# Kernel optimization log

Hardware: AMD Instinct MI355X
Metric: run time of the kernel (lower is better)

The kernel has to match this reference:

```python
import jax, jax.numpy as jnp
import numpy as np

B, N, M, DQ, DK, DV, H = 8, 1024, 1024, 512, 512, 512, 8
DH = DV // H           # per-head dim (dim_split)
DFF = 4 * DV           # FFN hidden dim
EPS = 1e-5


def _layernorm(x, g, b):
    mu = jnp.mean(x, axis=-1, keepdims=True)
    var = jnp.mean(jnp.square(x - mu), axis=-1, keepdims=True)
    return (x - mu) * jax.lax.rsqrt(var + EPS) * g + b


def setup_inputs() -> dict:
    key = jax.random.key(0)
    ks = jax.random.split(key, 20)
    s = 0.02
    return {
        "Q": jax.random.normal(ks[0], (B, N, DQ), jnp.float32),
        "K": jax.random.normal(ks[1], (B, M, DK), jnp.float32),
        "Wq": jax.random.normal(ks[2], (DV, DQ), jnp.float32) * s,
        "bq": jnp.zeros((DV,), jnp.float32),
        "Wk": jax.random.normal(ks[3], (DV, DK), jnp.float32) * s,
        "bk": jnp.zeros((DV,), jnp.float32),
        "Wv": jax.random.normal(ks[4], (DV, DK), jnp.float32) * s,
        "bv": jnp.zeros((DV,), jnp.float32),
        "W1": jax.random.normal(ks[5], (DFF, DV), jnp.float32) * s,
        "b1": jnp.zeros((DFF,), jnp.float32),
        "W2": jax.random.normal(ks[6], (DFF, DFF), jnp.float32) * s,
        "b2": jnp.zeros((DFF,), jnp.float32),
        "W3": jax.random.normal(ks[7], (DV, DFF), jnp.float32) * s,
        "b3": jnp.zeros((DV,), jnp.float32),
        "g0": jnp.ones((DV,), jnp.float32),
        "beta0": jnp.zeros((DV,), jnp.float32),
        "g1": jnp.ones((DV,), jnp.float32),
        "beta1": jnp.zeros((DV,), jnp.float32),
    }


def reference(Q, K, Wq, bq, Wk, bk, Wv, bv, W1, b1, W2, b2, W3, b3, g0, beta0, g1, beta1):
    # projections (torch Linear: x @ W.T + b)
    Qp = Q @ Wq.T + bq            # [B, N, DV]
    Kp = K @ Wk.T + bk            # [B, M, DV]
    Vp = K @ Wv.T + bv            # [B, M, DV]

    # split heads: [B, S, DV] -> [B, S, H, DH]
    Qh = Qp.reshape(B, N, H, DH)
    Kh = Kp.reshape(B, M, H, DH)
    Vh = Vp.reshape(B, M, H, DH)

    # scaled dot-product attention (scale = sqrt(head_dim))
    A = jnp.einsum("bnhd,bmhd->bhnm", Qh, Kh) / jnp.sqrt(jnp.float32(DH))
    A = jax.nn.softmax(A, axis=-1)
    O = jnp.einsum("bhnm,bmhd->bnhd", A, Vh).reshape(B, N, DV)

    # residual with projected Q, then LN
    O = _layernorm(O + Qp, g0, beta0)

    # FFN: Linear->ReLU->Linear->ReLU->Linear (num_hidden_layers=2)
    h = jax.nn.relu(O @ W1.T + b1)
    h = jax.nn.relu(h @ W2.T + b2)
    Off = h @ W3.T + b3

    return _layernorm(O + Off, g1, beta1)
```

## Files before the change

### kernel.cpp

```cpp
#include <hip/hip_runtime.h>


typedef __bf16 bf16_t;
typedef __bf16 bf16x8 __attribute__((ext_vector_type(8)));
typedef __bf16 bf16x4 __attribute__((ext_vector_type(4)));
typedef __bf16 bf16x2 __attribute__((ext_vector_type(2)));
typedef float  f32x4  __attribute__((ext_vector_type(4)));
typedef float  f32x16 __attribute__((ext_vector_type(16)));
typedef int    i32x4_t __attribute__((ext_vector_type(4)));
typedef int    i32x8_t __attribute__((ext_vector_type(8)));

__device__ __forceinline__ f32x4 mfma16(bf16x8 a, bf16x8 b, f32x4 c) {
  return __builtin_amdgcn_mfma_f32_16x16x32_bf16(a, b, c, 0, 0, 0);
}

__device__ __forceinline__ void gload_lds16(const void* g, void* l) {
  __builtin_amdgcn_global_load_lds((const __attribute__((address_space(1))) void*)g,
                                   (__attribute__((address_space(3))) void*)l,
                                   16, 0, 0);
}

__device__ __forceinline__ unsigned char to_fp8(float v) {
  return (unsigned char)(__builtin_amdgcn_cvt_pk_fp8_f32(v, v, 0, false) & 0xff);
}

__global__ __launch_bounds__(256) void cast_all(
    const float* __restrict__ Q, const float* __restrict__ K,
    const float* __restrict__ Wq, const float* __restrict__ Wk,
    const float* __restrict__ Wv, const float* __restrict__ W1,
    const float* __restrict__ W2, const float* __restrict__ W3,
    bf16_t* Qb, bf16_t* Kb, bf16_t* Wqb, bf16_t* Wkb, bf16_t* Wvb,
    unsigned char* W1q, unsigned char* W2q, unsigned char* W3q)
{
  long i = ((long)blockIdx.x * 256 + threadIdx.x) * 4;
  if (i >= 9175040L) {
    const float* s; unsigned char* d; long o;
    if      (i < 10223616L) { s = W1; d = W1q; o = i - 9175040L;  }
    else if (i < 14417920L) { s = W2; d = W2q; o = i - 10223616L; }
    else                    { s = W3; d = W3q; o = i - 14417920L; }
    float4 v = *(const float4*)(s + o);
    unsigned int lo = __builtin_amdgcn_cvt_pk_fp8_f32(v.x, v.y, 0, false);
    unsigned int hi = __builtin_amdgcn_cvt_pk_fp8_f32(v.z, v.w, 0, false);
    *(unsigned int*)(d + o) = (lo & 0xffffu) | (hi << 16);
    return;
  }
  const float* s; bf16_t* d; long o;
  if      (i <  4194304L) { s = Q;  d = Qb;  o = i;             }
  else if (i <  8388608L) { s = K;  d = Kb;  o = i - 4194304L;  }
  else if (i <  8650752L) { s = Wq; d = Wqb; o = i - 8388608L;  }
  else if (i <  8912896L) { s = Wk; d = Wkb; o = i - 8650752L;  }
  else                    { s = Wv; d = Wvb; o = i - 8912896L;  }
  float4 v = *(const float4*)(s + o);
  bf16x4 w;
  w[0] = (bf16_t)v.x; w[1] = (bf16_t)v.y; w[2] = (bf16_t)v.z; w[3] = (bf16_t)v.w;
  *(bf16x4*)(d + o) = w;
}

template <bool VTEPI>
__device__ __forceinline__ void gemm_core(
    const bf16_t* __restrict__ A, const bf16_t* __restrict__ W,
    const float* __restrict__ bias,
    bf16_t* __restrict__ Cb, bf16_t* __restrict__ VTout,
    float bscale, int N, int K, int lda, int ldb, int bx, int by)
{
  constexpr int FI = 4;
  constexpr int FJ = 4;
  constexpr int CN = 64;
  constexpr int SM_AB = 256 * 64 * 2;
  constexpr int SM_TS = 128 * 132 * 2;
  constexpr int SMEM = (VTEPI && SM_TS > SM_AB) ? SM_TS : SM_AB;

  __shared__ __align__(16) char smem[SMEM];

  const int tid  = threadIdx.x;
  const int wave = tid >> 6, lane = tid & 63;
  const int lq   = lane & 15, quad = lane >> 4;
  const int wm   = wave & 1;
  const int wn   = wave >> 1;
  const long row0 = (long)bx * 128;
  const long col0 = (long)by * 128;

  const int sr = tid >> 3;
  const int cg = (tid & 7) ^ (sr & 7);
  const bf16_t* ag = A + (row0 + sr) * (long)lda + cg * 8;
  const bf16_t* bg = W + (col0 + sr) * (long)ldb + cg * 8;
  const int asOff = wave * 1024;
  const int bsOff = 128 * 128 + wave * 1024;
  const long arows32 = 32L * lda;
  const long brows32 = 32L * ldb;

  auto stage = [&](int k0) {
#pragma unroll
    for (int is = 0; is < 4; is++)
      gload_lds16(ag + is * arows32 + k0, smem + asOff + is * 4096);
#pragma unroll
    for (int is = 0; is < 4; is++)
      gload_lds16(bg + is * brows32 + k0, smem + bsOff + is * 4096);
  };

  const int off0 = (quad ^ (lq & 7)) * 8;
  const int aO0 = ((wm * 64 + lq) * 64 + off0) * 2;
  const int aO1 = ((wm * 64 + lq) * 64 + (off0 ^ 32)) * 2;
  const int bO0 = 128 * 128 + ((wn * CN + lq) * 64 + off0) * 2;
  const int bO1 = 128 * 128 + ((wn * CN + lq) * 64 + (off0 ^ 32)) * 2;

  f32x4 acc[FI][FJ];
#pragma unroll
  for (int i = 0; i < FI; i++)
#pragma unroll
    for (int j = 0; j < FJ; j++) acc[i][j] = (f32x4){0.f, 0.f, 0.f, 0.f};

  const int nt = K >> 6;
  for (int t = 0; t < nt; ++t) {
    __syncthreads();
    stage(t * 64);
    __syncthreads();

    bf16x8 af[FI], bw[FJ];
#pragma unroll
    for (int i = 0; i < FI; i++) af[i] = *(const bf16x8*)(smem + aO0 + i * 2048);
#pragma unroll
    for (int j = 0; j < FJ; j++) bw[j] = *(const bf16x8*)(smem + bO0 + j * 2048);
#pragma unroll
    for (int i = 0; i < FI; i++)
#pragma unroll
      for (int j = 0; j < FJ; j++)
        acc[i][j] = mfma16(af[i], bw[j], acc[i][j]);
#pragma unroll
    for (int i = 0; i < FI; i++) af[i] = *(const bf16x8*)(smem + aO1 + i * 2048);
#pragma unroll
    for (int j = 0; j < FJ; j++) bw[j] = *(const bf16x8*)(smem + bO1 + j * 2048);
#pragma unroll
    for (int i = 0; i < FI; i++)
#pragma unroll
      for (int j = 0; j < FJ; j++)
        acc[i][j] = mfma16(af[i], bw[j], acc[i][j]);
  }

  float bc[FJ];
#pragma unroll
  for (int j = 0; j < FJ; j++)
    bc[j] = bias ? bias[col0 + wn * CN + j * 16 + lq] : 0.f;

  if (VTEPI && VTout) {
    bf16_t* Ts = (bf16_t*)smem;
    __syncthreads();
#pragma unroll
    for (int i = 0; i < FI; i++)
#pragma unroll
      for (int j = 0; j < FJ; j++) {
        bf16x4 pv;
#pragma unroll
        for (int r = 0; r < 4; r++) pv[r] = (bf16_t)(acc[i][j][r] + bc[j]);
        *(bf16x4*)(Ts + (wn * CN + j * 16 + lq) * 132 + wm * 64 + i * 16 + quad * 4) = pv;
      }
    __syncthreads();
    const int b  = bx >> 3;
    const int mb = (bx & 7) * 128;
    const int h0 = by * 2;
    const int dd = tid >> 4;
    const int mc = (tid & 15) * 8;
#pragma unroll
    for (int p = 0; p < 8; p++) {
      const int d = dd + p * 16;
      bf16x8 v = *(const bf16x8*)(Ts + d * 132 + mc);
      *(bf16x8*)(VTout + ((long)(b * 8 + h0 + (d >> 6))) * 65536
                 + (d & 63) * 1024 + mb + mc) = v;
    }
    return;
  }

  const long rb = row0 + wm * 64 + quad * 4;
  const long cb = col0 + wn * CN + lq;
#pragma unroll
  for (int i = 0; i < FI; i++)
#pragma unroll
    for (int j = 0; j < FJ; j++)
#pragma unroll
      for (int r = 0; r < 4; r++) {
        float v = acc[i][j][r] + bc[j];
        long idx = (rb + i * 16 + r) * (long)N + cb + j * 16;
        if (Cb) Cb[idx] = (bf16_t)(v * bscale);
      }
}

__global__ __launch_bounds__(256) void proj3(
    const bf16_t* __restrict__ Qb, const bf16_t* __restrict__ Kb,
    const bf16_t* __restrict__ Wqb, const bf16_t* __restrict__ Wkb,
    const bf16_t* __restrict__ Wvb,
    const float* __restrict__ bq, const float* __restrict__ bk,
    const float* __restrict__ bv,
    bf16_t* Qpb, bf16_t* Kpb, bf16_t* VT)
{
  const int z = blockIdx.z;
  const bf16_t* A  = (z == 0) ? Qb : Kb;
  const bf16_t* Wt = (z == 0) ? Wqb : ((z == 1) ? Wkb : Wvb);
  const float* bias = (z == 0) ? bq : ((z == 1) ? bk : bv);
  bf16_t* Cb = (z == 0) ? Qpb : ((z == 1) ? Kpb : nullptr);
  bf16_t* VTout = (z == 2) ? VT : nullptr;
  const float sc = (z == 1) ? 0.125f : 1.0f;
  gemm_core<true>(A, Wt, bias, Cb, VTout, sc,
                  512, 512, 512, 512, blockIdx.x, blockIdx.y);
}

template <int OUT, int BN>
__device__ __forceinline__ void fp8_gemm_core(
    const unsigned char* __restrict__ A, const unsigned char* __restrict__ B,
    const float* __restrict__ bias, unsigned char* __restrict__ C8,
    bf16_t* __restrict__ Cb, int ldab, int K, int koff, int N,
    int bxi, int byi)
{
  constexpr int NT = 2 * BN;
  constexpr int RPP = NT / 8;
  constexpr int A_P = 128 / RPP;
  constexpr int B_P = BN / RPP;
  constexpr int PASSB = NT * 16;

  __shared__ unsigned char As[16384];
  __shared__ unsigned char Bs[BN * 128];
  const int tid = threadIdx.x;
  const int wave = tid >> 6, lane = tid & 63;
  const int wm = wave & 1, wn = wave >> 1;
  const int m = lane & 31, h = lane >> 5;
  const long row0 = (long)bxi * 128;
  const long col0 = (long)byi * BN;

  const int sr = tid >> 3;
  const int cg = (tid & 7) ^ (sr & 7);
  const unsigned char* ag = A + (row0 + sr) * (long)ldab + koff + cg * 16;
  const unsigned char* bg = B + (col0 + sr) * (long)ldab + koff + cg * 16;
  char* asD = (char*)As + wave * 1024;
  char* bsD = (char*)Bs + wave * 1024;
  const long rowsPP = (long)RPP * ldab;

  const int ar0 = wm * 64 + m, ar1 = ar0 + 32;
  const int br0 = wn * 64 + m, br1 = wn * 64 + 32 + m;

  f32x16 acc[2][2];
#pragma unroll
  for (int mi = 0; mi < 2; mi++)
#pragma unroll
    for (int nj = 0; nj < 2; nj++)
#pragma unroll
      for (int r = 0; r < 16; r++) acc[mi][nj][r] = 0.f;

  for (int k0 = 0; k0 < K; k0 += 128) {
    __syncthreads();
#pragma unroll
    for (int is = 0; is < A_P; is++)
      gload_lds16(ag + is * rowsPP + k0, asD + is * PASSB);
#pragma unroll
    for (int is = 0; is < B_P; is++)
      gload_lds16(bg + is * rowsPP + k0, bsD + is * PASSB);
    __syncthreads();
#pragma unroll
    for (int ks = 0; ks < 2; ks++) {
      const int c0 = ks * 4 + h * 2;
      i32x8_t a[2], b[2];
#pragma unroll
      for (int mi = 0; mi < 2; mi++) {
        const int r = mi ? ar1 : ar0;
        i32x4_t lo = *(const i32x4_t*)(As + r * 128 + ((c0    ) ^ (r & 7)) * 16);
        i32x4_t hi = *(const i32x4_t*)(As + r * 128 + ((c0 + 1) ^ (r & 7)) * 16);
        a[mi][0] = lo[0]; a[mi][1] = lo[1]; a[mi][2] = lo[2]; a[mi][3] = lo[3];
        a[mi][4] = hi[0]; a[mi][5] = hi[1]; a[mi][6] = hi[2]; a[mi][7] = hi[3];
      }
#pragma unroll
      for (int nj = 0; nj < 2; nj++) {
        const int r = nj ? br1 : br0;
        i32x4_t lo = *(const i32x4_t*)(Bs + r * 128 + ((c0    ) ^ (r & 7)) * 16);
        i32x4_t hi = *(const i32x4_t*)(Bs + r * 128 + ((c0 + 1) ^ (r & 7)) * 16);
        b[nj][0] = lo[0]; b[nj][1] = lo[1]; b[nj][2] = lo[2]; b[nj][3] = lo[3];
        b[nj][4] = hi[0]; b[nj][5] = hi[1]; b[nj][6] = hi[2]; b[nj][7] = hi[3];
      }
#pragma unroll
      for (int mi = 0; mi < 2; mi++)
#pragma unroll
        for (int nj = 0; nj < 2; nj++)
          acc[mi][nj] = __builtin_amdgcn_mfma_scale_f32_32x32x64_f8f6f4(
              a[mi], b[nj], acc[mi][nj], 0, 0,
              0, 0x7f7f7f7f, 0, 0x7f7f7f7f);
    }
  }

  float bc[2];
  bc[0] = bias ? bias[col0 + wn * 64 + m] : 0.f;
  bc[1] = bias ? bias[col0 + wn * 64 + 32 + m] : 0.f;
#pragma unroll
  for (int mi = 0; mi < 2; mi++)
#pragma unroll
    for (int nj = 0; nj < 2; nj++)
#pragma unroll
      for (int reg = 0; reg < 16; reg++) {
        const int rl = (reg & 3) + 8 * (reg >> 2) + 4 * h;
        const long idx = (row0 + wm * 64 + mi * 32 + rl) * (long)N
                       + col0 + wn * 64 + nj * 32 + m;
        if (OUT == 0) {
          float v = fmaxf(acc[mi][nj][reg] + bc[nj], 0.f);
          C8[idx] = to_fp8(v);
        } else {
          Cb[idx] = (bf16_t)acc[mi][nj][reg];
        }
      }
}

__global__ __launch_bounds__(512) void ffn1_fp8(
    const unsigned char* __restrict__ Xq, const unsigned char* __restrict__ W1,
    const float* __restrict__ bias, unsigned char* __restrict__ C)
{
  fp8_gemm_core<0, 256>(Xq, W1, bias, C, nullptr, 512, 512, 0, 2048,
                        blockIdx.x, blockIdx.y);
}

__global__ __launch_bounds__(512) void ffn2_fp8(
    const unsigned char* __restrict__ H1, const unsigned char* __restrict__ W2,
    const float* __restrict__ bias, unsigned char* __restrict__ C)
{
  fp8_gemm_core<0, 256>(H1, W2, bias, C, nullptr, 2048, 2048, 0, 2048,
                        blockIdx.x, blockIdx.y);
}

__global__ __launch_bounds__(256) void ffn3_fp8(
    const unsigned char* __restrict__ H2, const unsigned char* __restrict__ W3,
    bf16_t* __restrict__ Off01)
{
  const int z = blockIdx.z;
  fp8_gemm_core<1, 128>(H2, W3, nullptr, nullptr, Off01 + (long)z * 4194304,
                        2048, 1024, z * 1024, 512, blockIdx.x, blockIdx.y);
}

__global__ __launch_bounds__(256) void attn(
    const bf16_t* __restrict__ Qp, const bf16_t* __restrict__ Kp,
    const bf16_t* __restrict__ VT, bf16_t* __restrict__ O)
{
  const int d0 = blockIdx.x;
  const int j  = d0 >> 3;
  const int g  = (d0 & 7) * 8 + (j >> 3);
  const int qb = j & 7;
  const int h  = g & 7, b = g >> 3;

  const int tid = threadIdx.x;
  const int wave = tid >> 6, lane = tid & 63;
  const int lq = lane & 15, quad = lane >> 4;

  __shared__ bf16_t Ks[2][8192];
  __shared__ bf16_t VTs[2][8192];
  __shared__ bf16_t Ps[4][16 * 72];

  const long bh = (long)b * 1024;
  const int qrowA = qb * 128 + wave * 16 + lq;
  const int qrowB = qrowA + 64;

  const bf16_t* qpA = Qp + (bh + qrowA) * 512 + h * 64 + quad * 8;
  const bf16_t* qpB = Qp + (bh + qrowB) * 512 + h * 64 + quad * 8;
  const bf16x8 qfA0 = *(const bf16x8*)qpA;
  const bf16x8 qfA1 = *(const bf16x8*)(qpA + 32);
  const bf16x8 qfB0 = *(const bf16x8*)qpB;
  const bf16x8 qfB1 = *(const bf16x8*)(qpB + 32);

  f32x4 oaccA[4], oaccB[4];
#pragma unroll
  for (int t = 0; t < 4; t++) {
    oaccA[t] = (f32x4){0.f, 0.f, 0.f, 0.f};
    oaccB[t] = (f32x4){0.f, 0.f, 0.f, 0.f};
  }
  float lA = 0.f, lB = 0.f;

  const int sr = tid >> 3;
  const int cg = (tid & 7) ^ (sr & 7);
  const bf16_t* kg  = Kp + bh * 512 + h * 64;
  const bf16_t* vtg = VT + ((long)b * 8 + h) * 65536;
  const int off0 = (quad ^ (lq & 7)) * 8;

  auto stage = [&](int m0, int bi) {
    char* ksDst = (char*)(Ks[bi]) + wave * 1024;
    char* vtDst = (char*)(VTs[bi]) + wave * 1024;
#pragma unroll
    for (int s = 0; s < 2; s++) {
      gload_lds16(kg + (long)(m0 + s * 64 + sr) * 512 + cg * 8,      ksDst + s * 8192);
      gload_lds16(kg + (long)(m0 + s * 64 + sr + 32) * 512 + cg * 8, ksDst + s * 8192 + 4096);
      gload_lds16(vtg + (long)sr * 1024 + m0 + s * 64 + cg * 8,        vtDst + s * 8192);
      gload_lds16(vtg + (long)(sr + 32) * 1024 + m0 + s * 64 + cg * 8, vtDst + s * 8192 + 4096);
    }
  };

  stage(0, 0);

  for (int t = 0; t < 8; ++t) {
    const int cur = t & 1;
    if (t < 7) {
      stage((t + 1) * 128, cur ^ 1);
      asm volatile("s_waitcnt vmcnt(8)" ::: "memory");
    } else {
      asm volatile("s_waitcnt vmcnt(0)" ::: "memory");
    }
    __builtin_amdgcn_s_barrier();
    __builtin_amdgcn_sched_barrier(0);

    const bf16_t* Kc = Ks[cur];
    const bf16_t* Vc = VTs[cur];

    f32x4 stA[8], stB[8];
#pragma unroll
    for (int tt = 0; tt < 8; tt++) {
      const bf16_t* kb = Kc + (tt >> 2) * 4096 + ((tt & 3) * 16 + lq) * 64;
      bf16x8 ka0 = *(const bf16x8*)(kb + off0);
      bf16x8 ka1 = *(const bf16x8*)(kb + (off0 ^ 32));
      f32x4 sA = (f32x4){0.f, 0.f, 0.f, 0.f};
      sA = mfma16(ka0, qfA0, sA);
      sA = mfma16(ka1, qfA1, sA);
      stA[tt] = sA;
      f32x4 sB = (f32x4){0.f, 0.f, 0.f, 0.f};
      sB = mfma16(ka0, qfB0, sB);
      sB = mfma16(ka1, qfB1, sB);
      stB[tt] = sB;
    }

    float lsA = 0.f, lsB = 0.f;
#pragma unroll
    for (int tt = 0; tt < 8; tt++)
#pragma unroll
      for (int r = 0; r < 4; r++) {
        float pA = __expf(stA[tt][r]);
        stA[tt][r] = pA;
        lsA += pA;
        float pB = __expf(stB[tt][r]);
        stB[tt][r] = pB;
        lsB += pB;
      }
    lsA += __shfl_xor(lsA, 16, 64);
    lsA += __shfl_xor(lsA, 32, 64);
    lA += lsA;
    lsB += __shfl_xor(lsB, 16, 64);
    lsB += __shfl_xor(lsB, 32, 64);
    lB += lsB;

    bf16_t* pw = &Ps[wave][0];
#pragma unroll
    for (int hh = 0; hh < 2; hh++) {
#pragma unroll
      for (int tt = 0; tt < 4; tt++) {
        bf16x4 pv;
#pragma unroll
        for (int r = 0; r < 4; r++) pv[r] = (bf16_t)stA[hh * 4 + tt][r];
        *(bf16x4*)(pw + lq * 72 + tt * 16 + quad * 4) = pv;
      }
#pragma unroll
      for (int ks = 0; ks < 2; ks++) {
        bf16x8 pb = *(const bf16x8*)(pw + lq * 72 + ks * 32 + quad * 8);
#pragma unroll
        for (int dt = 0; dt < 4; dt++) {
          const bf16_t* vb = Vc + hh * 4096 + (dt * 16 + lq) * 64;
          bf16x8 va = *(const bf16x8*)(vb + (ks ? (off0 ^ 32) : off0));
          oaccA[dt] = mfma16(va, pb, oaccA[dt]);
        }
      }
    }
#pragma unroll
    for (int hh = 0; hh < 2; hh++) {
#pragma unroll
      for (int tt = 0; tt < 4; tt++) {
        bf16x4 pv;
#pragma unroll
        for (int r = 0; r < 4; r++) pv[r] = (bf16_t)stB[hh * 4 + tt][r];
        *(bf16x4*)(pw + lq * 72 + tt * 16 + quad * 4) = pv;
      }
#pragma unroll
      for (int ks = 0; ks < 2; ks++) {
        bf16x8 pb = *(const bf16x8*)(pw + lq * 72 + ks * 32 + quad * 8);
#pragma unroll
        for (int dt = 0; dt < 4; dt++) {
          const bf16_t* vb = Vc + hh * 4096 + (dt * 16 + lq) * 64;
          bf16x8 va = *(const bf16x8*)(vb + (ks ? (off0 ^ 32) : off0));
          oaccB[dt] = mfma16(va, pb, oaccB[dt]);
        }
      }
    }

    __builtin_amdgcn_sched_barrier(0);
    __builtin_amdgcn_s_barrier();
  }

  const float invA = 1.f / lA;
  const float invB = 1.f / lB;
  bf16_t* opA = O + (bh + qrowA) * 512 + h * 64 + quad * 4;
  bf16_t* opB = O + (bh + qrowB) * 512 + h * 64 + quad * 4;
#pragma unroll
  for (int dt = 0; dt < 4; dt++) {
    bf16x4 vA, vB;
#pragma unroll
    for (int r = 0; r < 4; r++) {
      vA[r] = (bf16_t)(oaccA[dt][r] * invA);
      vB[r] = (bf16_t)(oaccB[dt][r] * invB);
    }
    *(bf16x4*)(opA + dt * 16) = vA;
    *(bf16x4*)(opB + dt * 16) = vB;
  }
}

__device__ __forceinline__ float2 ld2(const float* p, long row, int tid) {
  return ((const float2*)(p + row * 512))[tid];
}
__device__ __forceinline__ float2 ld2(const bf16_t* p, long row, int tid) {
  bf16x2 v = *(const bf16x2*)(p + row * 512 + tid * 2);
  return make_float2((float)v[0], (float)v[1]);
}

__device__ __forceinline__ void ln_finish(
    float x0, float x1, const float* g, const float* be, int tid,
    int wave, int lane, float* of, bf16_t* ob, unsigned char* o8, long row)
{
  float s = x0 + x1, ss = x0 * x0 + x1 * x1;
#pragma unroll
  for (int off = 1; off < 64; off <<= 1) {
    s  += __shfl_xor(s,  off, 64);
    ss += __shfl_xor(ss, off, 64);
  }
  __shared__ float sm[8];
  if (lane == 0) { sm[wave] = s; sm[4 + wave] = ss; }
  __syncthreads();
  s  = sm[0] + sm[1] + sm[2] + sm[3];
  ss = sm[4] + sm[5] + sm[6] + sm[7];
  const float mu = s * (1.f / 512.f);
  const float var = ss * (1.f / 512.f) - mu * mu;
  const float rs = rsqrtf(var + 1e-5f);
  const float2 gg = ((const float2*)g)[tid];
  const float2 bb = ((const float2*)be)[tid];
  const float o0 = (x0 - mu) * rs * gg.x + bb.x;
  const float o1 = (x1 - mu) * rs * gg.y + bb.y;
  if (of) ((float2*)(of + row * 512))[tid] = make_float2(o0, o1);
  if (ob) {
    bf16x2 t; t[0] = (bf16_t)o0; t[1] = (bf16_t)o1;
    *(bf16x2*)(ob + row * 512 + tid * 2) = t;
  }
  if (o8) {
    unsigned int p = __builtin_amdgcn_cvt_pk_fp8_f32(o0, o1, 0, false);
    *(unsigned short*)(o8 + row * 512 + tid * 2) = (unsigned short)(p & 0xffffu);
  }
}

__global__ __launch_bounds__(256) void ln_res(
    const bf16_t* __restrict__ A, const bf16_t* __restrict__ Bv,
    const float* __restrict__ g, const float* __restrict__ be,
    bf16_t* __restrict__ ob, unsigned char* __restrict__ o8)
{
  const int row = blockIdx.x, tid = threadIdx.x;
  const float2 va = ld2(A,  (long)row, tid);
  const float2 vb = ld2(Bv, (long)row, tid);
  ln_finish(va.x + vb.x, va.y + vb.y, g, be, tid, tid >> 6, tid & 63,
            nullptr, ob, o8, row);
}

__global__ __launch_bounds__(256) void ln_res3(
    const bf16_t* __restrict__ X, const bf16_t* __restrict__ O0,
    const bf16_t* __restrict__ O1, const float* __restrict__ bias,
    const float* __restrict__ g, const float* __restrict__ be,
    float* __restrict__ of)
{
  const int row = blockIdx.x, tid = threadIdx.x;
  const float2 vx = ld2(X,  (long)row, tid);
  const float2 v0 = ld2(O0, (long)row, tid);
  const float2 v1 = ld2(O1, (long)row, tid);
  const float2 vb = ((const float2*)bias)[tid];
  ln_finish(vx.x + v0.x + v1.x + vb.x, vx.y + v0.y + v1.y + vb.y,
            g, be, tid, tid >> 6, tid & 63, of, nullptr, nullptr, row);
}

extern "C" void kernel_launch(void* const* d_in, const int* in_sizes, int n_in,
                              void* d_out, int out_size, void* d_ws, size_t ws_size,
                              hipStream_t stream)
{
  const float* Q   = (const float*)d_in[0];
  const float* K   = (const float*)d_in[1];
  const float* Wq  = (const float*)d_in[2];
  const float* bq  = (const float*)d_in[3];
  const float* Wk  = (const float*)d_in[4];
  const float* bk  = (const float*)d_in[5];
  const float* Wv  = (const float*)d_in[6];
  const float* bv  = (const float*)d_in[7];
  const float* W1  = (const float*)d_in[8];
  const float* b1  = (const float*)d_in[9];
  const float* W2  = (const float*)d_in[10];
  const float* b2  = (const float*)d_in[11];
  const float* W3  = (const float*)d_in[12];
  const float* b3  = (const float*)d_in[13];
  const float* g0  = (const float*)d_in[14];
  const float* be0 = (const float*)d_in[15];
  const float* g1  = (const float*)d_in[16];
  const float* be1 = (const float*)d_in[17];

  char* ws = (char*)d_ws;
  bf16_t* Wqb = (bf16_t*)(ws + 0);
  bf16_t* Wkb = (bf16_t*)(ws + 524288);
  bf16_t* Wvb = (bf16_t*)(ws + 1048576);
  unsigned char* W1q = (unsigned char*)(ws + 1572864);
  unsigned char* W3q = (unsigned char*)(ws + 3670016);
  unsigned char* W2q = (unsigned char*)(ws + 5767168);
  bf16_t* Qb  = (bf16_t*)(ws + 14155776);
  bf16_t* Kb  = (bf16_t*)(ws + 22544384);
  bf16_t* Qpb = (bf16_t*)(ws + 30932992);
  bf16_t* Kpb = (bf16_t*)(ws + 39321600);
  bf16_t* VT  = (bf16_t*)(ws + 47710208);
  bf16_t* Of  = (bf16_t*)(ws + 14155776);
  bf16_t* Xb  = (bf16_t*)(ws + 22544384);
  unsigned char* Xq = (unsigned char*)(ws + 47710208);
  unsigned char* H2q = (unsigned char*)(ws + 30932992);
  unsigned char* H1q = (unsigned char*)(ws + 64487424);
  bf16_t* Off0 = (bf16_t*)(ws + 64487424);
  bf16_t* Off1 = (bf16_t*)(ws + 72876032);
  float*  out = (float*)d_out;

  cast_all<<<15104, 256, 0, stream>>>(Q, K, Wq, Wk, Wv, W1, W2, W3,
                                      Qb, Kb, Wqb, Wkb, Wvb, W1q, W2q, W3q);
  proj3<<<dim3(64, 4, 3), 256, 0, stream>>>(Qb, Kb, Wqb, Wkb, Wvb, bq, bk, bv,
                                            Qpb, Kpb, VT);
  attn<<<dim3(512, 1, 1), 256, 0, stream>>>(Qpb, Kpb, VT, Of);
  ln_res<<<8192, 256, 0, stream>>>(Of, Qpb, g0, be0, Xb, Xq);
  ffn1_fp8<<<dim3(64, 8), 512, 0, stream>>>(Xq, W1q, b1, H1q);
  ffn2_fp8<<<dim3(64, 8), 512, 0, stream>>>(H1q, W2q, b2, H2q);
  ffn3_fp8<<<dim3(64, 4, 2), 256, 0, stream>>>(H2q, W3q, Off0);
  ln_res3<<<8192, 256, 0, stream>>>(Xb, Off0, Off1, b3, g1, be1, out);
}
```

Baseline: 257.3 us.

## Double-buffer bf16 projection GEMM LDS staging and retile FFN1 to 128-column blocks

The bf16 GEMM core (used by the projections) now keeps two LDS buffers. It prefetches the next K-tile with global_load_lds while the current tile is consumed, and uses explicit vmcnt waits and barriers instead of two syncthreads per iteration. This aims to overlap global loads with MFMA work, at the cost of double the shared memory per block, which may reduce occupancy. Separately, FFN1 switches to a 128-wide tile with 256 threads and twice as many column blocks, for finer granularity on the small-K GEMM.

```diff
diff --git a/kernel.cpp b/kernel.cpp
--- a/kernel.cpp
+++ b/kernel.cpp
@@ -67,8 +67,7 @@
   constexpr int FJ = 4;
   constexpr int CN = 64;
   constexpr int SM_AB = 256 * 64 * 2;
-  constexpr int SM_TS = 128 * 132 * 2;
-  constexpr int SMEM = (VTEPI && SM_TS > SM_AB) ? SM_TS : SM_AB;
+  constexpr int SMEM = 2 * SM_AB;
 
   __shared__ __align__(16) char smem[SMEM];
 
@@ -89,13 +88,14 @@
   const long arows32 = 32L * lda;
   const long brows32 = 32L * ldb;
 
-  auto stage = [&](int k0) {
+  auto stage = [&](int k0, int bi) {
+    char* base = smem + bi * SM_AB;
 #pragma unroll
     for (int is = 0; is < 4; is++)
-      gload_lds16(ag + is * arows32 + k0, smem + asOff + is * 4096);
+      gload_lds16(ag + is * arows32 + k0, base + asOff + is * 4096);
 #pragma unroll
     for (int is = 0; is < 4; is++)
-      gload_lds16(bg + is * brows32 + k0, smem + bsOff + is * 4096);
+      gload_lds16(bg + is * brows32 + k0, base + bsOff + is * 4096);
   };
 
   const int off0 = (quad ^ (lq & 7)) * 8;
@@ -111,30 +111,41 @@
     for (int j = 0; j < FJ; j++) acc[i][j] = (f32x4){0.f, 0.f, 0.f, 0.f};
 
   const int nt = K >> 6;
+  stage(0, 0);
   for (int t = 0; t < nt; ++t) {
-    __syncthreads();
-    stage(t * 64);
-    __syncthreads();
+    const int cur = t & 1;
+    if (t < nt - 1) {
+      stage((t + 1) * 64, cur ^ 1);
+      asm volatile("s_waitcnt vmcnt(8)" ::: "memory");
+    } else {
+      asm volatile("s_waitcnt vmcnt(0)" ::: "memory");
+    }
+    __builtin_amdgcn_s_barrier();
+    __builtin_amdgcn_sched_barrier(0);
+    const char* base = smem + cur * SM_AB;
 
     bf16x8 af[FI], bw[FJ];
 #pragma unroll
-    for (int i = 0; i < FI; i++) af[i] = *(const bf16x8*)(smem + aO0 + i * 2048);
-#pragma unroll
-    for (int j = 0; j < FJ; j++) bw[j] = *(const bf16x8*)(smem + bO0 + j * 2048);
+    for (int i = 0; i < FI; i++) af[i] = *(const bf16x8*)(base + aO0 + i * 2048);
+#pragma unroll
+    for (int j = 0; j < FJ; j++) bw[j] = *(const bf16x8*)(base + bO0 + j * 2048);
 #pragma unroll
     for (int i = 0; i < FI; i++)
 #pragma unroll
       for (int j = 0; j < FJ; j++)
         acc[i][j] = mfma16(af[i], bw[j], acc[i][j]);
 #pragma unroll
-    for (int i = 0; i < FI; i++) af[i] = *(const bf16x8*)(smem + aO1 + i * 2048);
-#pragma unroll
-    for (int j = 0; j < FJ; j++) bw[j] = *(const bf16x8*)(smem + bO1 + j * 2048);
+    for (int i = 0; i < FI; i++) af[i] = *(const bf16x8*)(base + aO1 + i * 2048);
+#pragma unroll
+    for (int j = 0; j < FJ; j++) bw[j] = *(const bf16x8*)(base + bO1 + j * 2048);
 #pragma unroll
     for (int i = 0; i < FI; i++)
 #pragma unroll
       for (int j = 0; j < FJ; j++)
         acc[i][j] = mfma16(af[i], bw[j], acc[i][j]);
+
+    __builtin_amdgcn_sched_barrier(0);
+    __builtin_amdgcn_s_barrier();
   }
 
   float bc[FJ];
@@ -304,11 +315,11 @@
       }
 }
 
-__global__ __launch_bounds__(512) void ffn1_fp8(
+__global__ __launch_bounds__(256) void ffn1_fp8(
     const unsigned char* __restrict__ Xq, const unsigned char* __restrict__ W1,
     const float* __restrict__ bias, unsigned char* __restrict__ C)
 {
-  fp8_gemm_core<0, 256>(Xq, W1, bias, C, nullptr, 512, 512, 0, 2048,
+  fp8_gemm_core<0, 128>(Xq, W1, bias, C, nullptr, 512, 512, 0, 2048,
                         blockIdx.x, blockIdx.y);
 }
 
@@ -616,7 +627,7 @@
                                             Qpb, Kpb, VT);
   attn<<<dim3(512, 1, 1), 256, 0, stream>>>(Qpb, Kpb, VT, Of);
   ln_res<<<8192, 256, 0, stream>>>(Of, Qpb, g0, be0, Xb, Xq);
-  ffn1_fp8<<<dim3(64, 8), 512, 0, stream>>>(Xq, W1q, b1, H1q);
+  ffn1_fp8<<<dim3(64, 16), 256, 0, stream>>>(Xq, W1q, b1, H1q);
   ffn2_fp8<<<dim3(64, 8), 512, 0, stream>>>(H1q, W2q, b2, H2q);
   ffn3_fp8<<<dim3(64, 4, 2), 256, 0, stream>>>(H2q, W3q, Off0);
   ln_res3<<<8192, 256, 0, stream>>>(Xb, Off0, Off1, b3, g1, be1, out);
```

After: 250.9 us. -2.5%, faster.
